# Performance work log

Measured on AMD Instinct MI355X. Metric: run time of the kernel, lower is better.

Reference implementation:

```python
import jax, jax.numpy as jnp
import numpy as np
from jax import lax

PAD = 40
MAX_DISP = 40
STRIDE2 = 1
CORR_MULT = 1.0


def _correlation1d(input1, input2):
    # input1, input2: [B, C, H, W]; kernel_size=1, stride1=1
    B, C, H, W = input1.shape
    D = 2 * MAX_DISP // STRIDE2 + 1  # 81 displacement channels
    # zero-pad input2 along the width dimension
    in2p = jnp.pad(input2, ((0, 0), (0, 0), (0, 0), (PAD, PAD)))
    offsets = jnp.arange(D, dtype=jnp.int32) * STRIDE2  # start col in padded map; disp = off - PAD

    def body(carry, off):
        shifted = lax.dynamic_slice(in2p, (0, 0, 0, off), (B, C, H, W))
        # mean over channels (sumelems = kernel_size^2 * C = C)
        c = jnp.sum(input1 * shifted, axis=1) / C  # [B, H, W]
        return carry, c

    _, corr = lax.scan(body, None, offsets)  # [D, B, H, W]
    out = jnp.transpose(corr, (1, 0, 2, 3)) * CORR_MULT  # [B, D, H, W]
    return out


def setup_inputs() -> dict:
    key = jax.random.key(0)
    k1, k2 = jax.random.split(key)
    input1 = jax.random.normal(k1, (8, 256, 96, 192), dtype=jnp.float32)
    input2 = jax.random.normal(k2, (8, 256, 96, 192), dtype=jnp.float32)
    return {"input1": input1, "input2": input2}


def reference(input1, input2):
    return _correlation1d(input1, input2)
```

## Files before the change

### kernel.cpp

```cpp
#include <hip/hip_runtime.h>


typedef __attribute__((ext_vector_type(8))) short short8;
typedef __attribute__((ext_vector_type(4))) short short4v;
typedef __attribute__((ext_vector_type(4))) float float4v;

#if defined(__has_builtin)
#if __has_builtin(__builtin_amdgcn_mfma_f32_16x16x16bf16_1k)
#define HAVE_MFMA16 1
#endif
#endif
#ifndef HAVE_MFMA16
#define HAVE_MFMA16 0
#endif

__device__ __forceinline__ unsigned short f2bf(float f) {
  unsigned int u = __float_as_uint(f);
  return (unsigned short)((u + 0x7FFFu + ((u >> 16) & 1u)) >> 16);
}

__global__ __launch_bounds__(256, 3) void corr1d_kernel(
    const float* __restrict__ in1, const float* __restrict__ in2,
    float* __restrict__ out) {
  constexpr int W = 192, H = 96, C = 256, D = 81;
  constexpr int HW = H * W;
  constexpr int KC = 16;
  constexpr int SR = 196;
  constexpr int ES = 196;
  constexpr int BUF = KC * SR;

  __shared__ __align__(16) float smem[4 * BUF];
  float* E = smem;

  const int bh = blockIdx.x;
  const int b = bh / H, h = bh % H;
  const int tid = threadIdx.x;
  const int lane = tid & 63;
  const int wv = tid >> 6;
  const int l15 = lane & 15, lq = lane >> 4;
  const int base = (b * C * H + h) * W;

  float4v acc[3][6];
#pragma unroll
  for (int i = 0; i < 3; ++i)
#pragma unroll
    for (int jj = 0; jj < 6; ++jj) acc[i][jj] = (float4v){0.f, 0.f, 0.f, 0.f};

  int soff[3], loff[3];
#pragma unroll
  for (int g = 0; g < 3; ++g) {
    const int fidx = 256 * g + 4 * lane;
    const int r = fidx / 192;
    const int col = fidx - 192 * r;
    soff[g] = (4 * wv + r) * HW + col;
    loff[g] = (4 * wv + r) * SR + col;
  }
  const float* in1p = in1 + base;
  const float* in2p = in2 + base;

  float4v rA0[3], rB0[3], rA1[3], rB1[3];
  auto LOAD0 = [&](int m) {
    const float* g1 = in1p + KC * m * HW;
    const float* g2 = in2p + KC * m * HW;
#pragma unroll
    for (int g = 0; g < 3; ++g) {
      rA0[g] = *(const float4v*)(g1 + soff[g]);
      rB0[g] = *(const float4v*)(g2 + soff[g]);
    }
  };
  auto LOAD1 = [&](int m) {
    const float* g1 = in1p + KC * m * HW;
    const float* g2 = in2p + KC * m * HW;
#pragma unroll
    for (int g = 0; g < 3; ++g) {
      rA1[g] = *(const float4v*)(g1 + soff[g]);
      rB1[g] = *(const float4v*)(g2 + soff[g]);
    }
  };
  auto WRITE0 = [&]() {
    float* As = smem;
    float* Bs = smem + BUF;
#pragma unroll
    for (int g = 0; g < 3; ++g) {
      *(float4v*)(As + loff[g]) = rA0[g];
      *(float4v*)(Bs + loff[g]) = rB0[g];
    }
  };
  auto WRITE1 = [&]() {
    float* As = smem + 2 * BUF;
    float* Bs = smem + 3 * BUF;
#pragma unroll
    for (int g = 0; g < 3; ++g) {
      *(float4v*)(As + loff[g]) = rA1[g];
      *(float4v*)(Bs + loff[g]) = rB1[g];
    }
  };

  auto compute_chunk = [&](int p) {
    const float* As = smem + p * (2 * BUF);
    const float* Bs = As + BUF;
#if HAVE_MFMA16
    short4v af[3];
#pragma unroll
    for (int i = 0; i < 3; ++i) {
      const float* ap = As + 48 * wv + 16 * i + l15;
      unsigned short o[4];
#pragma unroll
      for (int t = 0; t < 4; ++t) o[t] = f2bf(ap[(4 * lq + t) * SR]);
      af[i] = *(const short4v*)o;
    }
#pragma unroll
    for (int jt = 0; jt < 8; ++jt) {
      const int j = 16 * (3 * wv + jt) + l15;
      const bool ok = (j >= 40) && (j < 232);
      const float* bp = Bs + (ok ? (j - 40) : 0);
      unsigned short o[4];
#pragma unroll
      for (int t = 0; t < 4; ++t) {
        float v = ok ? bp[(4 * lq + t) * SR] : 0.0f;
        o[t] = f2bf(v);
      }
      short4v bfr = *(const short4v*)o;
#pragma unroll
      for (int i = 0; i < 3; ++i) {
        const int jj = jt - i;
        if (jj >= 0 && jj < 6)
          acc[i][jj] = __builtin_amdgcn_mfma_f32_16x16x16bf16_1k(
              af[i], bfr, acc[i][jj], 0, 0, 0);
      }
    }
#else
    const bool okq = (lq < 2);
    const int rb = okq ? 8 * lq : 0;
    short8 af[3];
#pragma unroll
    for (int i = 0; i < 3; ++i) {
      const float* ap = As + 48 * wv + 16 * i + l15;
      unsigned short o[8];
#pragma unroll
      for (int t = 0; t < 8; ++t) {
        float v = ap[(rb + t) * SR];
        o[t] = okq ? f2bf(v) : (unsigned short)0;
      }
      af[i] = *(const short8*)o;
    }
#pragma unroll
    for (int jt = 0; jt < 8; ++jt) {
      const int j = 16 * (3 * wv + jt) + l15;
      const bool ok = (j >= 40) && (j < 232);
      const float* bp = Bs + (ok ? (j - 40) : 0);
      unsigned short o[8];
#pragma unroll
      for (int t = 0; t < 8; ++t) {
        float v = bp[(rb + t) * SR];
        o[t] = (ok && okq) ? f2bf(v) : (unsigned short)0;
      }
      short8 bfr = *(const short8*)o;
#pragma unroll
      for (int i = 0; i < 3; ++i) {
        const int jj = jt - i;
        if (jj >= 0 && jj < 6)
          acc[i][jj] = __builtin_amdgcn_mfma_f32_16x16x32_bf16(
              af[i], bfr, acc[i][jj], 0, 0, 0);
      }
    }
#endif
  };

  LOAD0(0);
  LOAD1(1);
  asm volatile("s_waitcnt vmcnt(6)" ::: "memory");
  WRITE0();
  LOAD0(2);
  asm volatile("s_waitcnt lgkmcnt(0)" ::: "memory");
  __builtin_amdgcn_s_barrier();
#pragma unroll 1
  for (int t = 0; t < 7; ++t) {
    const int m = 2 * t;
    compute_chunk(0);
    __builtin_amdgcn_s_barrier();
    asm volatile("s_waitcnt vmcnt(6)" ::: "memory");
    WRITE1();
    if (m + 3 < 16) LOAD1(m + 3);
    asm volatile("s_waitcnt lgkmcnt(0)" ::: "memory");
    __builtin_amdgcn_s_barrier();
    compute_chunk(1);
    __builtin_amdgcn_s_barrier();
    asm volatile("s_waitcnt vmcnt(6)" ::: "memory");
    WRITE0();
    if (m + 4 < 16) LOAD0(m + 4);
    asm volatile("s_waitcnt lgkmcnt(0)" ::: "memory");
    __builtin_amdgcn_s_barrier();
  }
  compute_chunk(0);
  __builtin_amdgcn_s_barrier();
  asm volatile("s_waitcnt vmcnt(0)" ::: "memory");
  WRITE1();
  asm volatile("s_waitcnt lgkmcnt(0)" ::: "memory");
  __builtin_amdgcn_s_barrier();
  compute_chunk(1);

  const float scale = 1.0f / 256.0f;
#pragma unroll
  for (int p = 0; p < 2; ++p) {
    const int dlo = p ? 41 : 0;
    const int nd  = p ? 40 : 41;
    __syncthreads();
#pragma unroll
    for (int i = 0; i < 3; ++i)
#pragma unroll
      for (int jj = 0; jj < 6; ++jj)
#pragma unroll
        for (int r = 0; r < 4; ++r) {
          const int d = 16 * jj + l15 - 4 * lq - r;
          const int w = 48 * wv + 16 * i + 4 * lq + r;
          if (d >= dlo && d < dlo + nd)
            E[(d - dlo) * ES + w] = acc[i][jj][r] * scale;
        }
    __syncthreads();
    for (int t = tid; t < nd * 48; t += 256) {
      const int dr = t / 48, g = t % 48;
      float4v val = *(const float4v*)(E + dr * ES + 4 * g);
      *(float4v*)(out + ((b * D + dlo + dr) * H + h) * W + 4 * g) = val;
    }
  }
}

extern "C" void kernel_launch(void* const* d_in, const int* in_sizes, int n_in,
                              void* d_out, int out_size, void* d_ws, size_t ws_size,
                              hipStream_t stream) {
  const float* in1 = (const float*)d_in[0];
  const float* in2 = (const float*)d_in[1];
  float* out = (float*)d_out;
  (void)in_sizes; (void)n_in; (void)out_size; (void)d_ws; (void)ws_size;
  corr1d_kernel<<<dim3(768), dim3(256), 0, stream>>>(in1, in2, out);
}
```

Measured before the change: 331.9 us.

## Split block into producer and consumer waves synchronized by LDS counters

```diff
diff --git a/kernel.cpp b/kernel.cpp
--- a/kernel.cpp
+++ b/kernel.cpp
@@ -19,7 +19,7 @@
   return (unsigned short)((u + 0x7FFFu + ((u >> 16) & 1u)) >> 16);
 }
 
-__global__ __launch_bounds__(256, 3) void corr1d_kernel(
+__global__ __launch_bounds__(512, 6) void corr1d_kernel(
     const float* __restrict__ in1, const float* __restrict__ in2,
     float* __restrict__ out) {
   constexpr int W = 192, H = 96, C = 256, D = 81;
@@ -30,175 +30,209 @@
   constexpr int BUF = KC * SR;
 
   __shared__ __align__(16) float smem[4 * BUF];
+  __shared__ int fullCnt[2];
+  __shared__ int freeCnt[2];
   float* E = smem;
 
   const int bh = blockIdx.x;
   const int b = bh / H, h = bh % H;
   const int tid = threadIdx.x;
   const int lane = tid & 63;
-  const int wv = tid >> 6;
+  const int wid = tid >> 6;
   const int l15 = lane & 15, lq = lane >> 4;
   const int base = (b * C * H + h) * W;
 
+  if (tid < 2) { fullCnt[tid] = 0; freeCnt[tid] = 0; }
+  __syncthreads();
+
   float4v acc[3][6];
-#pragma unroll
-  for (int i = 0; i < 3; ++i)
-#pragma unroll
-    for (int jj = 0; jj < 6; ++jj) acc[i][jj] = (float4v){0.f, 0.f, 0.f, 0.f};
-
-  int soff[3], loff[3];
-#pragma unroll
-  for (int g = 0; g < 3; ++g) {
-    const int fidx = 256 * g + 4 * lane;
-    const int r = fidx / 192;
-    const int col = fidx - 192 * r;
-    soff[g] = (4 * wv + r) * HW + col;
-    loff[g] = (4 * wv + r) * SR + col;
+
+  if (wid >= 4) {
+    const int pv = wid - 4;
+    int soff[3], loff[3];
+#pragma unroll
+    for (int g = 0; g < 3; ++g) {
+      const int fidx = 256 * g + 4 * lane;
+      const int r = fidx / 192;
+      const int col = fidx - 192 * r;
+      soff[g] = (4 * pv + r) * HW + col;
+      loff[g] = (4 * pv + r) * SR + col;
+    }
+    const float* in1p = in1 + base;
+    const float* in2p = in2 + base;
+
+    float4v rA0[3], rB0[3], rA1[3], rB1[3];
+    auto LOAD0 = [&](int m) {
+      const float* g1 = in1p + KC * m * HW;
+      const float* g2 = in2p + KC * m * HW;
+#pragma unroll
+      for (int g = 0; g < 3; ++g) {
+        rA0[g] = *(const float4v*)(g1 + soff[g]);
+        rB0[g] = *(const float4v*)(g2 + soff[g]);
+      }
+    };
+    auto LOAD1 = [&](int m) {
+      const float* g1 = in1p + KC * m * HW;
+      const float* g2 = in2p + KC * m * HW;
+#pragma unroll
+      for (int g = 0; g < 3; ++g) {
+        rA1[g] = *(const float4v*)(g1 + soff[g]);
+        rB1[g] = *(const float4v*)(g2 + soff[g]);
+      }
+    };
+    auto WRITE0 = [&]() {
+      float* As = smem;
+      float* Bs = smem + BUF;
+#pragma unroll
+      for (int g = 0; g < 3; ++g) {
+        *(float4v*)(As + loff[g]) = rA0[g];
+        *(float4v*)(Bs + loff[g]) = rB0[g];
+      }
+    };
+    auto WRITE1 = [&]() {
+      float* As = smem + 2 * BUF;
+      float* Bs = smem + 3 * BUF;
+#pragma unroll
+      for (int g = 0; g < 3; ++g) {
+        *(float4v*)(As + loff[g]) = rA1[g];
+        *(float4v*)(Bs + loff[g]) = rB1[g];
+      }
+    };
+    auto waitFree = [&](int m) {
+      const int need = 4 * (m >> 1);
+      if (need > 0) {
+        while (__hip_atomic_load(&freeCnt[m & 1], __ATOMIC_ACQUIRE,
+                                 __HIP_MEMORY_SCOPE_WORKGROUP) < need)
+          __builtin_amdgcn_s_sleep(1);
+      }
+      __builtin_amdgcn_sched_barrier(0);
+    };
+    auto signalFull = [&](int p) {
+      asm volatile("s_waitcnt lgkmcnt(0)" ::: "memory");
+      if (lane == 0)
+        __hip_atomic_fetch_add(&fullCnt[p], 1, __ATOMIC_RELEASE,
+                               __HIP_MEMORY_SCOPE_WORKGROUP);
+    };
+
+    LOAD0(0);
+    LOAD1(1);
+#pragma unroll 1
+    for (int t = 0; t < 7; ++t) {
+      const int m = 2 * t;
+      asm volatile("s_waitcnt vmcnt(6)" ::: "memory");
+      waitFree(m);
+      WRITE0(); signalFull(0);
+      LOAD0(m + 2);
+      asm volatile("s_waitcnt vmcnt(6)" ::: "memory");
+      waitFree(m + 1);
+      WRITE1(); signalFull(1);
+      if (m + 3 < 16) LOAD1(m + 3);
+    }
+    asm volatile("s_waitcnt vmcnt(6)" ::: "memory");
+    waitFree(14); WRITE0(); signalFull(0);
+    asm volatile("s_waitcnt vmcnt(0)" ::: "memory");
+    waitFree(15); WRITE1(); signalFull(1);
+  } else {
+    const int wv = wid;
+#pragma unroll
+    for (int i = 0; i < 3; ++i)
+#pragma unroll
+      for (int jj = 0; jj < 6; ++jj) acc[i][jj] = (float4v){0.f, 0.f, 0.f, 0.f};
+
+    auto compute_chunk = [&](int p) {
+      const float* As = smem + p * (2 * BUF);
+      const float* Bs = As + BUF;
+#if HAVE_MFMA16
+      short4v af[3];
+#pragma unroll
+      for (int i = 0; i < 3; ++i) {
+        const float* ap = As + 48 * wv + 16 * i + l15;
+        unsigned short o[4];
+#pragma unroll
+        for (int t = 0; t < 4; ++t) o[t] = f2bf(ap[(4 * lq + t) * SR]);
+        af[i] = *(const short4v*)o;
+      }
+#pragma unroll
+      for (int jt = 0; jt < 8; ++jt) {
+        const int j = 16 * (3 * wv + jt) + l15;
+        const bool ok = (j >= 40) && (j < 232);
+        const float* bp = Bs + (ok ? (j - 40) : 0);
+        unsigned short o[4];
+#pragma unroll
+        for (int t = 0; t < 4; ++t) {
+          float v = ok ? bp[(4 * lq + t) * SR] : 0.0f;
+          o[t] = f2bf(v);
+        }
+        short4v bfr = *(const short4v*)o;
+#pragma unroll
+        for (int i = 0; i < 3; ++i) {
+          const int jj = jt - i;
+          if (jj >= 0 && jj < 6)
+            acc[i][jj] = __builtin_amdgcn_mfma_f32_16x16x16bf16_1k(
+                af[i], bfr, acc[i][jj], 0, 0, 0);
+        }
+      }
+#else
+      const bool okq = (lq < 2);
+      const int rb = okq ? 8 * lq : 0;
+      short8 af[3];
+#pragma unroll
+      for (int i = 0; i < 3; ++i) {
+        const float* ap = As + 48 * wv + 16 * i + l15;
+        unsigned short o[8];
+#pragma unroll
+        for (int t = 0; t < 8; ++t) {
+          float v = ap[(rb + t) * SR];
+          o[t] = okq ? f2bf(v) : (unsigned short)0;
+        }
+        af[i] = *(const short8*)o;
+      }
+#pragma unroll
+      for (int jt = 0; jt < 8; ++jt) {
+        const int j = 16 * (3 * wv + jt) + l15;
+        const bool ok = (j >= 40) && (j < 232);
+        const float* bp = Bs + (ok ? (j - 40) : 0);
+        unsigned short o[8];
+#pragma unroll
+        for (int t = 0; t < 8; ++t) {
+          float v = bp[(rb + t) * SR];
+          o[t] = (ok && okq) ? f2bf(v) : (unsigned short)0;
+        }
+        short8 bfr = *(const short8*)o;
+#pragma unroll
+        for (int i = 0; i < 3; ++i) {
+          const int jj = jt - i;
+          if (jj >= 0 && jj < 6)
+            acc[i][jj] = __builtin_amdgcn_mfma_f32_16x16x32_bf16(
+                af[i], bfr, acc[i][jj], 0, 0, 0);
+        }
+      }
+#endif
+    };
+    auto waitFull = [&](int m) {
+      const int need = 4 * (m >> 1) + 4;
+      while (__hip_atomic_load(&fullCnt[m & 1], __ATOMIC_ACQUIRE,
+                               __HIP_MEMORY_SCOPE_WORKGROUP) < need)
+        __builtin_amdgcn_s_sleep(1);
+      __builtin_amdgcn_sched_barrier(0);
+    };
+    auto signalFree = [&](int p) {
+      asm volatile("s_waitcnt lgkmcnt(0)" ::: "memory");
+      if (lane == 0)
+        __hip_atomic_fetch_add(&freeCnt[p], 1, __ATOMIC_RELEASE,
+                               __HIP_MEMORY_SCOPE_WORKGROUP);
+    };
+
+#pragma unroll 1
+    for (int t = 0; t < 8; ++t) {
+      waitFull(2 * t);
+      compute_chunk(0);
+      signalFree(0);
+      waitFull(2 * t + 1);
+      compute_chunk(1);
+      signalFree(1);
+    }
   }
-  const float* in1p = in1 + base;
-  const float* in2p = in2 + base;
-
-  float4v rA0[3], rB0[3], rA1[3], rB1[3];
-  auto LOAD0 = [&](int m) {
-    const float* g1 = in1p + KC * m * HW;
-    const float* g2 = in2p + KC * m * HW;
-#pragma unroll
-    for (int g = 0; g < 3; ++g) {
-      rA0[g] = *(const float4v*)(g1 + soff[g]);
-      rB0[g] = *(const float4v*)(g2 + soff[g]);
-    }
-  };
-  auto LOAD1 = [&](int m) {
-    const float* g1 = in1p + KC * m * HW;
-    const float* g2 = in2p + KC * m * HW;
-#pragma unroll
-    for (int g = 0; g < 3; ++g) {
-      rA1[g] = *(const float4v*)(g1 + soff[g]);
-      rB1[g] = *(const float4v*)(g2 + soff[g]);
-    }
-  };
-  auto WRITE0 = [&]() {
-    float* As = smem;
-    float* Bs = smem + BUF;
-#pragma unroll
-    for (int g = 0; g < 3; ++g) {
-      *(float4v*)(As + loff[g]) = rA0[g];
-      *(float4v*)(Bs + loff[g]) = rB0[g];
-    }
-  };
-  auto WRITE1 = [&]() {
-    float* As = smem + 2 * BUF;
-    float* Bs = smem + 3 * BUF;
-#pragma unroll
-    for (int g = 0; g < 3; ++g) {
-      *(float4v*)(As + loff[g]) = rA1[g];
-      *(float4v*)(Bs + loff[g]) = rB1[g];
-    }
-  };
-
-  auto compute_chunk = [&](int p) {
-    const float* As = smem + p * (2 * BUF);
-    const float* Bs = As + BUF;
-#if HAVE_MFMA16
-    short4v af[3];
-#pragma unroll
-    for (int i = 0; i < 3; ++i) {
-      const float* ap = As + 48 * wv + 16 * i + l15;
-      unsigned short o[4];
-#pragma unroll
-      for (int t = 0; t < 4; ++t) o[t] = f2bf(ap[(4 * lq + t) * SR]);
-      af[i] = *(const short4v*)o;
-    }
-#pragma unroll
-    for (int jt = 0; jt < 8; ++jt) {
-      const int j = 16 * (3 * wv + jt) + l15;
-      const bool ok = (j >= 40) && (j < 232);
-      const float* bp = Bs + (ok ? (j - 40) : 0);
-      unsigned short o[4];
-#pragma unroll
-      for (int t = 0; t < 4; ++t) {
-        float v = ok ? bp[(4 * lq + t) * SR] : 0.0f;
-        o[t] = f2bf(v);
-      }
-      short4v bfr = *(const short4v*)o;
-#pragma unroll
-      for (int i = 0; i < 3; ++i) {
-        const int jj = jt - i;
-        if (jj >= 0 && jj < 6)
-          acc[i][jj] = __builtin_amdgcn_mfma_f32_16x16x16bf16_1k(
-              af[i], bfr, acc[i][jj], 0, 0, 0);
-      }
-    }
-#else
-    const bool okq = (lq < 2);
-    const int rb = okq ? 8 * lq : 0;
-    short8 af[3];
-#pragma unroll
-    for (int i = 0; i < 3; ++i) {
-      const float* ap = As + 48 * wv + 16 * i + l15;
-      unsigned short o[8];
-#pragma unroll
-      for (int t = 0; t < 8; ++t) {
-        float v = ap[(rb + t) * SR];
-        o[t] = okq ? f2bf(v) : (unsigned short)0;
-      }
-      af[i] = *(const short8*)o;
-    }
-#pragma unroll
-    for (int jt = 0; jt < 8; ++jt) {
-      const int j = 16 * (3 * wv + jt) + l15;
-      const bool ok = (j >= 40) && (j < 232);
-      const float* bp = Bs + (ok ? (j - 40) : 0);
-      unsigned short o[8];
-#pragma unroll
-      for (int t = 0; t < 8; ++t) {
-        float v = bp[(rb + t) * SR];
-        o[t] = (ok && okq) ? f2bf(v) : (unsigned short)0;
-      }
-      short8 bfr = *(const short8*)o;
-#pragma unroll
-      for (int i = 0; i < 3; ++i) {
-        const int jj = jt - i;
-        if (jj >= 0 && jj < 6)
-          acc[i][jj] = __builtin_amdgcn_mfma_f32_16x16x32_bf16(
-              af[i], bfr, acc[i][jj], 0, 0, 0);
-      }
-    }
-#endif
-  };
-
-  LOAD0(0);
-  LOAD1(1);
-  asm volatile("s_waitcnt vmcnt(6)" ::: "memory");
-  WRITE0();
-  LOAD0(2);
-  asm volatile("s_waitcnt lgkmcnt(0)" ::: "memory");
-  __builtin_amdgcn_s_barrier();
-#pragma unroll 1
-  for (int t = 0; t < 7; ++t) {
-    const int m = 2 * t;
-    compute_chunk(0);
-    __builtin_amdgcn_s_barrier();
-    asm volatile("s_waitcnt vmcnt(6)" ::: "memory");
-    WRITE1();
-    if (m + 3 < 16) LOAD1(m + 3);
-    asm volatile("s_waitcnt lgkmcnt(0)" ::: "memory");
-    __builtin_amdgcn_s_barrier();
-    compute_chunk(1);
-    __builtin_amdgcn_s_barrier();
-    asm volatile("s_waitcnt vmcnt(6)" ::: "memory");
-    WRITE0();
-    if (m + 4 < 16) LOAD0(m + 4);
-    asm volatile("s_waitcnt lgkmcnt(0)" ::: "memory");
-    __builtin_amdgcn_s_barrier();
-  }
-  compute_chunk(0);
-  __builtin_amdgcn_s_barrier();
-  asm volatile("s_waitcnt vmcnt(0)" ::: "memory");
-  WRITE1();
-  asm volatile("s_waitcnt lgkmcnt(0)" ::: "memory");
-  __builtin_amdgcn_s_barrier();
-  compute_chunk(1);
 
   const float scale = 1.0f / 256.0f;
 #pragma unroll
@@ -206,19 +240,22 @@
     const int dlo = p ? 41 : 0;
     const int nd  = p ? 40 : 41;
     __syncthreads();
-#pragma unroll
-    for (int i = 0; i < 3; ++i)
-#pragma unroll
-      for (int jj = 0; jj < 6; ++jj)
-#pragma unroll
-        for (int r = 0; r < 4; ++r) {
-          const int d = 16 * jj + l15 - 4 * lq - r;
-          const int w = 48 * wv + 16 * i + 4 * lq + r;
-          if (d >= dlo && d < dlo + nd)
-            E[(d - dlo) * ES + w] = acc[i][jj][r] * scale;
-        }
+    if (wid < 4) {
+      const int wv = wid;
+#pragma unroll
+      for (int i = 0; i < 3; ++i)
+#pragma unroll
+        for (int jj = 0; jj < 6; ++jj)
+#pragma unroll
+          for (int r = 0; r < 4; ++r) {
+            const int d = 16 * jj + l15 - 4 * lq - r;
+            const int w = 48 * wv + 16 * i + 4 * lq + r;
+            if (d >= dlo && d < dlo + nd)
+              E[(d - dlo) * ES + w] = acc[i][jj][r] * scale;
+          }
+    }
     __syncthreads();
-    for (int t = tid; t < nd * 48; t += 256) {
+    for (int t = tid; t < nd * 48; t += 512) {
       const int dr = t / 48, g = t % 48;
       float4v val = *(const float4v*)(E + dr * ES + 4 * g);
       *(float4v*)(out + ((b * D + dlo + dr) * H + h) * W + 4 * g) = val;
@@ -233,5 +270,5 @@
   const float* in2 = (const float*)d_in[1];
   float* out = (float*)d_out;
   (void)in_sizes; (void)n_in; (void)out_size; (void)d_ws; (void)ws_size;
-  corr1d_kernel<<<dim3(768), dim3(256), 0, stream>>>(in1, in2, out);
+  corr1d_kernel<<<dim3(768), dim3(512), 0, stream>>>(in1, in2, out);
 }
```

Measured after the change: 446.1 us. 1.34x slower.
